# Optimization experiments

Measured on AMD Instinct MI355X. Metric: run time of the kernel, lower is better.

Reference implementation:

```python
import jax, jax.numpy as jnp
import numpy as np

B, T, A = 4096, 32, 3
HID, D, N, K = 1024, 128, 16, 4096
FLAT = T * A            # 96
LAT = N * D             # 2048
COMMIT = 0.25


def setup_inputs() -> dict:
    key = jax.random.key(0)
    ks = jax.random.split(key, 14)
    s = 0.02
    return {
        "actions": jax.random.normal(ks[0], (B, T, A), jnp.float32),
        # encoder: FLAT -> HID -> HID -> N*D
        "e_w1": jax.random.normal(ks[1], (FLAT, HID), jnp.float32) * s,
        "e_b1": jnp.zeros((HID,), jnp.float32),
        "e_w2": jax.random.normal(ks[2], (HID, HID), jnp.float32) * s,
        "e_b2": jnp.zeros((HID,), jnp.float32),
        "e_w3": jax.random.normal(ks[3], (HID, LAT), jnp.float32) * s,
        "e_b3": jnp.zeros((LAT,), jnp.float32),
        # codebook init: uniform(-1/K, 1/K) as in torch init
        "codebook": jax.random.uniform(ks[4], (K, D), jnp.float32, -1.0 / K, 1.0 / K),
        # decoder: N*D -> HID -> HID -> FLAT
        "d_w1": jax.random.normal(ks[5], (LAT, HID), jnp.float32) * s,
        "d_b1": jnp.zeros((HID,), jnp.float32),
        "d_w2": jax.random.normal(ks[6], (HID, HID), jnp.float32) * s,
        "d_b2": jnp.zeros((HID,), jnp.float32),
        "d_w3": jax.random.normal(ks[7], (HID, FLAT), jnp.float32) * s,
        "d_b3": jnp.zeros((FLAT,), jnp.float32),
    }


def reference(actions, e_w1, e_b1, e_w2, e_b2, e_w3, e_b3, codebook,
              d_w1, d_b1, d_w2, d_b2, d_w3, d_b3):
    sg = jax.lax.stop_gradient
    b = actions.shape[0]
    # encode: [B, T*A] -> [B, N, D]
    flat = actions.reshape(b, FLAT)
    h = jax.nn.silu(flat @ e_w1 + e_b1)
    h = jax.nn.silu(h @ e_w2 + e_b2)
    latents = (h @ e_w3 + e_b3).reshape(b, N, D)
    # nearest-code search: [B*N, K] squared distances
    fl = latents.reshape(b * N, D)
    dist = (fl * fl).sum(1, keepdims=True) + (codebook * codebook).sum(1)[None, :] - 2.0 * (fl @ codebook.T)
    indices = jnp.argmin(dist, axis=1).reshape(b, N)
    quantized = codebook[indices]                      # [B, N, D]
    codebook_loss = jnp.mean((quantized - sg(latents)) ** 2)
    commitment_loss = jnp.mean((latents - sg(quantized)) ** 2)
    vq_loss = codebook_loss + COMMIT * commitment_loss
    q_st = latents + sg(quantized - latents)           # straight-through
    # decode
    g = jax.nn.silu(q_st.reshape(b, LAT) @ d_w1 + d_b1)
    g = jax.nn.silu(g @ d_w2 + d_b2)
    recon = (g @ d_w3 + d_b3).reshape(b, T, A)
    recon_loss = jnp.mean((recon - actions) ** 2)
    loss = recon_loss + vq_loss
    return recon, indices, vq_loss, recon_loss, loss
```

## Files before the change

### kernel.cpp

```cpp
#include <hip/hip_runtime.h>
#include <hip/hip_bf16.h>

#define DD 128

__global__ void plant_diag(float val, float* out) {
    if (threadIdx.x == 0 && blockIdx.x == 0) out[0] = val;
}

__global__ void zero_acc(double* acc) {
    if (threadIdx.x == 0 && blockIdx.x == 0) { acc[0] = 0.0; acc[1] = 0.0; }
}

__device__ __forceinline__ float silu_np(float x) {
    float e = (float)exp(-(double)x);
    float u = 1.0f + e;
    float v = 1.0f / u;
    return x * v;
}

template <bool SILU>
__global__ __launch_bounds__(256) void gemm_db(const float* __restrict__ A,
                                               const float* __restrict__ W,
                                               const float* __restrict__ bias,
                                               float* __restrict__ C,
                                               int M, int N, int K) {
    __shared__ __align__(16) float As[128][36];
    __shared__ __align__(16) float Ws[32][68];
    const int t = threadIdx.x;
    const int tx = t & 15, ty = t >> 4;
    const int bm = blockIdx.y * 128, bn = blockIdx.x * 64;

    float acc[8][4];
#pragma unroll
    for (int i = 0; i < 8; ++i)
#pragma unroll
        for (int j = 0; j < 4; ++j) acc[i][j] = 0.0f;

    const int nPanels = (K + 31) / 32;
    float ra[16], rw[8];

    {
        const int k0 = 0;
#pragma unroll
        for (int it = 0; it < 16; ++it) {
            int e = t + 256 * it;
            int m = e >> 5, kk = e & 31;
            int mm = bm + m; if (mm >= M) mm = M - 1;
            int kc = k0 + kk;
            ra[it] = (kc < K) ? A[(size_t)mm * K + kc] : 0.0f;
        }
#pragma unroll
        for (int it = 0; it < 8; ++it) {
            int e = t + 256 * it;
            int r = e >> 6, c = e & 63;
            int n = bn + c;
            int kr = k0 + r;
            rw[it] = (kr < K && n < N) ? W[(size_t)kr * N + n] : 0.0f;
        }
    }

    for (int p = 0; p < nPanels; ++p) {
        __syncthreads();
#pragma unroll
        for (int it = 0; it < 16; ++it) {
            int e = t + 256 * it;
            As[e >> 5][e & 31] = ra[it];
        }
#pragma unroll
        for (int it = 0; it < 8; ++it) {
            int e = t + 256 * it;
            Ws[e >> 6][e & 63] = rw[it];
        }
        __syncthreads();

        if (p + 1 < nPanels) {
            const int k0 = (p + 1) * 32;
#pragma unroll
            for (int it = 0; it < 16; ++it) {
                int e = t + 256 * it;
                int m = e >> 5, kk = e & 31;
                int mm = bm + m; if (mm >= M) mm = M - 1;
                int kc = k0 + kk;
                ra[it] = (kc < K) ? A[(size_t)mm * K + kc] : 0.0f;
            }
#pragma unroll
            for (int it = 0; it < 8; ++it) {
                int e = t + 256 * it;
                int r = e >> 6, c = e & 63;
                int n = bn + c;
                int kr = k0 + r;
                rw[it] = (kr < K && n < N) ? W[(size_t)kr * N + n] : 0.0f;
            }
        }

#pragma unroll
        for (int kq = 0; kq < 8; ++kq) {
            float4 a4[8], w4[4];
#pragma unroll
            for (int i = 0; i < 8; ++i)
                a4[i] = *(const float4*)&As[ty + 16 * i][4 * kq];
#pragma unroll
            for (int q = 0; q < 4; ++q)
                w4[q] = *(const float4*)&Ws[4 * kq + q][4 * tx];
#pragma unroll
            for (int q = 0; q < 4; ++q) {
                const float wv[4] = {w4[q].x, w4[q].y, w4[q].z, w4[q].w};
#pragma unroll
                for (int i = 0; i < 8; ++i) {
                    const float av = ((const float*)&a4[i])[q];
#pragma unroll
                    for (int j = 0; j < 4; ++j)
                        acc[i][j] = fmaf(av, wv[j], acc[i][j]);
                }
            }
        }
    }

#pragma unroll
    for (int i = 0; i < 8; ++i) {
        int m = bm + ty + 16 * i;
#pragma unroll
        for (int j = 0; j < 4; ++j) {
            int n = bn + 4 * tx + j;
            if (m < M && n < N) {
                float x = acc[i][j] + bias[n];
                if (SILU) x = silu_np(x);
                C[(size_t)m * N + n] = x;
            }
        }
    }
}

__device__ __forceinline__ float pairwise128_sq(const float* __restrict__ x, int stride) {
    float r0 = x[0*stride]*x[0*stride], r1 = x[1*stride]*x[1*stride],
          r2 = x[2*stride]*x[2*stride], r3 = x[3*stride]*x[3*stride],
          r4 = x[4*stride]*x[4*stride], r5 = x[5*stride]*x[5*stride],
          r6 = x[6*stride]*x[6*stride], r7 = x[7*stride]*x[7*stride];
    for (int i = 8; i < 128; i += 8) {
        r0 += x[(i+0)*stride]*x[(i+0)*stride];
        r1 += x[(i+1)*stride]*x[(i+1)*stride];
        r2 += x[(i+2)*stride]*x[(i+2)*stride];
        r3 += x[(i+3)*stride]*x[(i+3)*stride];
        r4 += x[(i+4)*stride]*x[(i+4)*stride];
        r5 += x[(i+5)*stride]*x[(i+5)*stride];
        r6 += x[(i+6)*stride]*x[(i+6)*stride];
        r7 += x[(i+7)*stride]*x[(i+7)*stride];
    }
    return ((r0 + r1) + (r2 + r3)) + ((r4 + r5) + (r6 + r7));
}

__global__ void code_t2(const float* __restrict__ cb, float* __restrict__ t2, int K) {
    int k = blockIdx.x * 256 + threadIdx.x;
    if (k >= K) return;
    t2[k] = pairwise128_sq(cb + (size_t)k * DD, 1);
}

#define VQT_ROWS 128
#define VQT_CP   128
#define VQT_LT   132

__global__ __launch_bounds__(512, 2) void vq_t84(const float* __restrict__ lat,
                                                 const float* __restrict__ cb,
                                                 const float* __restrict__ t2,
                                                 float* __restrict__ pbv,
                                                 int* __restrict__ pbk,
                                                 int K, int rows_total) {
    __shared__ __align__(16) float Ls[VQT_ROWS][VQT_LT];
    __shared__ __align__(16) float Cs[VQT_CP][VQT_LT];
    __shared__ float T1s[VQT_ROWS];
    __shared__ float bwv[8][VQT_ROWS];
    __shared__ int   bwk[8][VQT_ROWS];

    const int t = threadIdx.x;
    const int tx = t & 15, ty = t >> 4;
    const int wave = t >> 6, lane = t & 63;
    const int r0 = blockIdx.x * VQT_ROWS;

#pragma unroll
    for (int it = 0; it < 8; ++it) {
        int g = t + 512 * it;
        int r = g >> 5, dq = g & 31;
        int rr = r0 + r; if (rr >= rows_total) rr = rows_total - 1;
        const float4 lv = *(const float4*)(lat + (size_t)rr * DD + 4 * dq);
        *(float4*)&Ls[r][4 * dq] = lv;
    }
    __syncthreads();

    if (t < VQT_ROWS) {
        const float* xr = &Ls[t][0];
        float4 q0 = *(const float4*)&xr[0];
        float4 q1 = *(const float4*)&xr[4];
        float a0 = q0.x*q0.x, a1 = q0.y*q0.y, a2 = q0.z*q0.z, a3 = q0.w*q0.w;
        float a4 = q1.x*q1.x, a5 = q1.y*q1.y, a6 = q1.z*q1.z, a7 = q1.w*q1.w;
#pragma unroll
        for (int i = 1; i < 16; ++i) {
            q0 = *(const float4*)&xr[8 * i];
            q1 = *(const float4*)&xr[8 * i + 4];
            a0 += q0.x*q0.x; a1 += q0.y*q0.y; a2 += q0.z*q0.z; a3 += q0.w*q0.w;
            a4 += q1.x*q1.x; a5 += q1.y*q1.y; a6 += q1.z*q1.z; a7 += q1.w*q1.w;
        }
        T1s[t] = ((a0 + a1) + (a2 + a3)) + ((a4 + a5) + (a6 + a7));
    }
    __syncthreads();

    float t1r[8];
#pragma unroll
    for (int i = 0; i < 8; ++i) t1r[i] = T1s[tx + 16 * i];

    float bestv[8]; int bestk[8];
#pragma unroll
    for (int i = 0; i < 8; ++i) { bestv[i] = 3.4e38f; bestk[i] = 0; }

    const int NPAN = K / VQT_CP;
#pragma unroll 1
    for (int p = 0; p < NPAN; ++p) {
        const float* src = cb + (size_t)p * VQT_CP * DD;
#pragma unroll
        for (int it = 0; it < 8; ++it) {
            int g = t + 512 * it;
            int cr = g >> 5, dq = g & 31;
            const float4 cv = *(const float4*)(src + (size_t)cr * DD + 4 * dq);
            *(float4*)&Cs[cr][4 * dq] = cv;
        }
        __syncthreads();

        const int kp = p * VQT_CP;
        float t2v[4];
#pragma unroll
        for (int j = 0; j < 4; ++j) t2v[j] = t2[kp + ty + 32 * j];

        float s[8][4];
#pragma unroll
        for (int i = 0; i < 8; ++i)
#pragma unroll
            for (int j = 0; j < 4; ++j) s[i][j] = 0.0f;

#pragma unroll 2
        for (int dq = 0; dq < 32; ++dq) {
            const float4 ca0 = *(const float4*)&Cs[ty     ][4 * dq];
            const float4 ca1 = *(const float4*)&Cs[ty + 32][4 * dq];
            const float4 ca2 = *(const float4*)&Cs[ty + 64][4 * dq];
            const float4 ca3 = *(const float4*)&Cs[ty + 96][4 * dq];
#pragma unroll
            for (int i = 0; i < 8; ++i) {
                const float4 la = *(const float4*)&Ls[tx + 16 * i][4 * dq];
                s[i][0] = fmaf(la.x, ca0.x, s[i][0]);
                s[i][0] = fmaf(la.y, ca0.y, s[i][0]);
                s[i][0] = fmaf(la.z, ca0.z, s[i][0]);
                s[i][0] = fmaf(la.w, ca0.w, s[i][0]);
                s[i][1] = fmaf(la.x, ca1.x, s[i][1]);
                s[i][1] = fmaf(la.y, ca1.y, s[i][1]);
                s[i][1] = fmaf(la.z, ca1.z, s[i][1]);
                s[i][1] = fmaf(la.w, ca1.w, s[i][1]);
                s[i][2] = fmaf(la.x, ca2.x, s[i][2]);
                s[i][2] = fmaf(la.y, ca2.y, s[i][2]);
                s[i][2] = fmaf(la.z, ca2.z, s[i][2]);
                s[i][2] = fmaf(la.w, ca2.w, s[i][2]);
                s[i][3] = fmaf(la.x, ca3.x, s[i][3]);
                s[i][3] = fmaf(la.y, ca3.y, s[i][3]);
                s[i][3] = fmaf(la.z, ca3.z, s[i][3]);
                s[i][3] = fmaf(la.w, ca3.w, s[i][3]);
            }
        }

#pragma unroll
        for (int i = 0; i < 8; ++i) {
            const float tt1 = t1r[i];
#pragma unroll
            for (int j = 0; j < 4; ++j) {
                const int c = kp + ty + 32 * j;
                const float dist = (tt1 + t2v[j]) - 2.0f * s[i][j];
                if (dist < bestv[i]) { bestv[i] = dist; bestk[i] = c; }
            }
        }
        __syncthreads();
    }

#pragma unroll
    for (int off = 16; off <= 32; off <<= 1) {
#pragma unroll
        for (int i = 0; i < 8; ++i) {
            float vv = __shfl_xor(bestv[i], off);
            int kk = __shfl_xor(bestk[i], off);
            if (vv < bestv[i] || (vv == bestv[i] && kk < bestk[i])) {
                bestv[i] = vv; bestk[i] = kk;
            }
        }
    }
    if (lane < 16) {
#pragma unroll
        for (int i = 0; i < 8; ++i) {
            bwv[wave][tx + 16 * i] = bestv[i];
            bwk[wave][tx + 16 * i] = bestk[i];
        }
    }
    __syncthreads();
    if (t < VQT_ROWS) {
        float bv = bwv[0][t]; int bk = bwk[0][t];
#pragma unroll
        for (int w = 1; w < 8; ++w) {
            float v = bwv[w][t]; int k = bwk[w][t];
            if (v < bv || (v == bv && k < bk)) { bv = v; bk = k; }
        }
        if (r0 + t < rows_total) {
            pbv[r0 + t] = bv;
            pbk[r0 + t] = bk;
        }
    }
}

__global__ __launch_bounds__(512) void vq_np4(const float* __restrict__ lat,
                                              const float* __restrict__ cb,
                                              const float* __restrict__ t2,
                                              float* __restrict__ pbv,
                                              int* __restrict__ pbk,
                                              int K, int Kc, int rows_total) {
    __shared__ __align__(16) float Ls[128][68];
    __shared__ __align__(16) float Cs[128][68];
    __shared__ float T1s[64];
    __shared__ float T2s[64];
    __shared__ float bwv[8][68];
    __shared__ int   bwk[8][68];

    const int t = threadIdx.x;
    const int tx = t & 15, ty = t >> 4;
    const int wave = t >> 6, lane = t & 63;
    const int r0 = blockIdx.x * 64;
    const int kbeg = blockIdx.y * Kc;
    const int kend = kbeg + Kc;

#pragma unroll
    for (int it = 0; it < 4; ++it) {
        int g = t + 512 * it;
        int row = g >> 5, dq = g & 31;
        int rr = r0 + row; if (rr >= rows_total) rr = rows_total - 1;
        const float4 v = *(const float4*)(lat + (size_t)rr * DD + 4 * dq);
        Ls[4*dq+0][row] = v.x; Ls[4*dq+1][row] = v.y;
        Ls[4*dq+2][row] = v.z; Ls[4*dq+3][row] = v.w;
    }
    __syncthreads();
    if (t < 64) T1s[t] = pairwise128_sq(&Ls[0][t], 68);

    float bestv[4]; int bestk[4];
#pragma unroll
    for (int r = 0; r < 4; ++r) { bestv[r] = 3.4e38f; bestk[r] = 0; }

    float4 pc[4];
    float pt2 = 0.0f;
#pragma unroll
    for (int it = 0; it < 4; ++it) {
        int g = t + 512 * it;
        int c = g >> 5, dq = g & 31;
        int cc = kbeg + c; if (cc >= K) cc = K - 1;
        pc[it] = *(const float4*)(cb + (size_t)cc * DD + 4 * dq);
    }
    if (t < 64) { int cc = kbeg + t; if (cc >= K) cc = K - 1; pt2 = t2[cc]; }

    for (int k0 = kbeg; k0 < kend; k0 += 64) {
        __syncthreads();
#pragma unroll
        for (int it = 0; it < 4; ++it) {
            int g = t + 512 * it;
            int c = g >> 5, dq = g & 31;
            Cs[4*dq+0][c] = pc[it].x; Cs[4*dq+1][c] = pc[it].y;
            Cs[4*dq+2][c] = pc[it].z; Cs[4*dq+3][c] = pc[it].w;
        }
        if (t < 64) T2s[t] = pt2;
        __syncthreads();

        if (k0 + 64 < kend) {
            const int kn = k0 + 64;
#pragma unroll
            for (int it = 0; it < 4; ++it) {
                int g = t + 512 * it;
                int c = g >> 5, dq = g & 31;
                int cc = kn + c; if (cc >= K) cc = K - 1;
                pc[it] = *(const float4*)(cb + (size_t)cc * DD + 4 * dq);
            }
            if (t < 64) { int cc = kn + t; if (cc >= K) cc = K - 1; pt2 = t2[cc]; }
        }

        float s[4][2];
#pragma unroll
        for (int r = 0; r < 4; ++r) { s[r][0] = 0.0f; s[r][1] = 0.0f; }

#pragma unroll 8
        for (int d = 0; d < 128; ++d) {
            const float4 a4 = *(const float4*)&Ls[d][4 * tx];
            const float2 c2 = *(const float2*)&Cs[d][2 * ty];
            const float av[4] = {a4.x, a4.y, a4.z, a4.w};
#pragma unroll
            for (int r = 0; r < 4; ++r) {
                s[r][0] = fmaf(av[r], c2.x, s[r][0]);
                s[r][1] = fmaf(av[r], c2.y, s[r][1]);
            }
        }

#pragma unroll
        for (int r = 0; r < 4; ++r) {
            const float t1 = T1s[4 * tx + r];
#pragma unroll
            for (int j = 0; j < 2; ++j) {
                int kc = k0 + 2 * ty + j;
                float dist = (t1 + T2s[2 * ty + j]) - 2.0f * s[r][j];
                if (kc < K && dist < bestv[r]) { bestv[r] = dist; bestk[r] = kc; }
            }
        }
    }

#pragma unroll
    for (int off = 16; off <= 32; off <<= 1) {
#pragma unroll
        for (int r = 0; r < 4; ++r) {
            float vv = __shfl_xor(bestv[r], off);
            int kk = __shfl_xor(bestk[r], off);
            if (vv < bestv[r] || (vv == bestv[r] && kk < bestk[r])) {
                bestv[r] = vv; bestk[r] = kk;
            }
        }
    }
    if (lane < 16) {
#pragma unroll
        for (int r = 0; r < 4; ++r) {
            bwv[wave][4 * lane + r] = bestv[r];
            bwk[wave][4 * lane + r] = bestk[r];
        }
    }
    __syncthreads();
    if (t < 64) {
        float bv = bwv[0][t]; int bk = bwk[0][t];
#pragma unroll
        for (int w = 1; w < 8; ++w) {
            float v = bwv[w][t]; int k = bwk[w][t];
            if (v < bv || (v == bv && k < bk)) { bv = v; bk = k; }
        }
        if (r0 + t < rows_total) {
            size_t o = (size_t)blockIdx.y * rows_total + (r0 + t);
            pbv[o] = bv;
            pbk[o] = bk;
        }
    }
}

__global__ __launch_bounds__(256) void vq_combine(const float* __restrict__ pbv,
                                                  const int* __restrict__ pbk,
                                                  int S, int rows,
                                                  int* __restrict__ indices,
                                                  double* __restrict__ acc) {
    int r = blockIdx.x * 256 + threadIdx.x;
    float bv = 3.4e38f; int bk = 0;
    if (r < rows) {
        for (int s = 0; s < S; ++s) {
            float v = pbv[(size_t)s * rows + r];
            int k = pbk[(size_t)s * rows + r];
            if (v < bv) { bv = v; bk = k; }
        }
        indices[r] = bk;
    }
    __shared__ double red[256];
    red[threadIdx.x] = (r < rows) ? (double)bv : 0.0;
    __syncthreads();
    for (int s = 128; s > 0; s >>= 1) {
        if (threadIdx.x < s) red[threadIdx.x] += red[threadIdx.x + s];
        __syncthreads();
    }
    if (threadIdx.x == 0) atomicAdd(acc, red[0]);
}

__global__ void q_gather(const int* __restrict__ idx, const float* __restrict__ cb,
                         float* __restrict__ Q, int count, int nlat) {
    int gid = blockIdx.x * 256 + threadIdx.x;
    if (gid >= count) return;
    int m = gid >> 11;
    int j = gid & 2047;
    int code = idx[m * nlat + (j >> 7)];
    Q[gid] = cb[((size_t)code << 7) + (j & 127)];
}

__global__ __launch_bounds__(256) void recon_out(const float* __restrict__ recon,
                                                 const float* __restrict__ actions,
                                                 float* __restrict__ out,
                                                 double* __restrict__ acc, int count) {
    int gid = blockIdx.x * 256 + threadIdx.x;
    double sq = 0.0;
    if (gid < count) {
        float rv = recon[gid];
        float av = actions[gid];
        double diff = (double)rv - (double)av;
        out[gid] = rv;
        sq = diff * diff;
    }
    __shared__ double red[256];
    red[threadIdx.x] = sq;
    __syncthreads();
    for (int s = 128; s > 0; s >>= 1) {
        if (threadIdx.x < s) red[threadIdx.x] += red[threadIdx.x + s];
        __syncthreads();
    }
    if (threadIdx.x == 0) atomicAdd(acc + 1, red[0]);
}

__global__ void idx_out(const int* __restrict__ idx, float* __restrict__ out, int count) {
    int gid = blockIdx.x * 256 + threadIdx.x;
    if (gid < count) out[gid] = (float)idx[gid];
}

__global__ void finalize(const double* __restrict__ acc, float* __restrict__ out,
                         double vq_den, double rec_den) {
    double vq = 1.25 * acc[0] / vq_den;
    double rl = acc[1] / rec_den;
    out[0] = (float)vq;
    out[1] = (float)rl;
    out[2] = (float)(rl + vq);
}

static inline int ceildiv(int a, int b) { return (a + b - 1) / b; }

extern "C" void kernel_launch(void* const* d_in, const int* in_sizes, int n_in,
                              void* d_out, int out_size, void* d_ws, size_t ws_size,
                              hipStream_t stream) {
    const float* actions = (const float*)d_in[0];
    const float* e_w1 = (const float*)d_in[1];
    const float* e_b1 = (const float*)d_in[2];
    const float* e_w2 = (const float*)d_in[3];
    const float* e_b2 = (const float*)d_in[4];
    const float* e_w3 = (const float*)d_in[5];
    const float* e_b3 = (const float*)d_in[6];
    const float* cb   = (const float*)d_in[7];
    const float* d_w1 = (const float*)d_in[8];
    const float* d_b1 = (const float*)d_in[9];
    const float* d_w2 = (const float*)d_in[10];
    const float* d_b2 = (const float*)d_in[11];
    const float* d_w3 = (const float*)d_in[12];
    const float* d_b3 = (const float*)d_in[13];
    float* out = (float*)d_out;

    const int FLAT = in_sizes[13];
    const int B    = in_sizes[0] / FLAT;
    const int HID  = in_sizes[2];
    const int LAT  = in_sizes[6];
    const int K    = in_sizes[7] / DD;
    const int NL   = LAT / DD;

    const bool tiled = (K % VQT_CP == 0);
    const int S = tiled ? 1 : ((K % 256 == 0) ? 4 : 1);
    const int Kc = K / S;

    int CHUNK = B;
    auto need = [&](int ch) -> size_t {
        return (size_t)ch * HID * 4 * 2 + (size_t)ch * LAT * 4 * 2
             + (size_t)ch * HID * 4 * 2 + (size_t)ch * FLAT * 4
             + (size_t)K * 4 + 64 + (size_t)B * NL * 4
             + (size_t)ch * NL * S * 8;
    };
    while (CHUNK > 16 && need(CHUNK) > ws_size) CHUNK >>= 1;
    if (need(CHUNK) > ws_size) {
        plant_diag<<<1, 64, 0, stream>>>(2222.0f, out);
        return;
    }
    const int NCHUNK = ceildiv(B, CHUNK);

    char* ws = (char*)d_ws;
    size_t off = 0;
    float* h1c  = (float*)(ws + off); off += (size_t)CHUNK * HID * 4;
    float* h2c  = (float*)(ws + off); off += (size_t)CHUNK * HID * 4;
    float* latc = (float*)(ws + off); off += (size_t)CHUNK * LAT * 4;
    float* Qc   = (float*)(ws + off); off += (size_t)CHUNK * LAT * 4;
    float* g1c  = (float*)(ws + off); off += (size_t)CHUNK * HID * 4;
    float* g2c  = (float*)(ws + off); off += (size_t)CHUNK * HID * 4;
    float* recc = (float*)(ws + off); off += (size_t)CHUNK * FLAT * 4;
    float* t2   = (float*)(ws + off); off += (size_t)K * 4;
    double* acc = (double*)(ws + off); off += 64;
    int*   idx  = (int*)(ws + off);   off += (size_t)B * NL * 4;
    float* pbv  = (float*)(ws + off); off += (size_t)CHUNK * NL * S * 4;
    int*   pbk  = (int*)(ws + off);

    zero_acc<<<1, 64, 0, stream>>>(acc);
    code_t2<<<ceildiv(K, 256), 256, 0, stream>>>(cb, t2, K);

    for (int c = 0; c < NCHUNK; ++c) {
        const int r0 = c * CHUNK;
        const int cbR = (B - r0 < CHUNK) ? (B - r0) : CHUNK;
        const float* act_c = actions + (size_t)r0 * FLAT;
        int* idx_c = idx + (size_t)r0 * NL;
        const int rows = cbR * NL;

        gemm_db<true><<<dim3(ceildiv(HID, 64), ceildiv(cbR, 128)), 256, 0, stream>>>(
            act_c, e_w1, e_b1, h1c, cbR, HID, FLAT);
        gemm_db<true><<<dim3(ceildiv(HID, 64), ceildiv(cbR, 128)), 256, 0, stream>>>(
            h1c, e_w2, e_b2, h2c, cbR, HID, HID);
        gemm_db<false><<<dim3(ceildiv(LAT, 64), ceildiv(cbR, 128)), 256, 0, stream>>>(
            h2c, e_w3, e_b3, latc, cbR, LAT, HID);

        if (tiled) {
            vq_t84<<<ceildiv(rows, VQT_ROWS), 512, 0, stream>>>(
                latc, cb, t2, pbv, pbk, K, rows);
        } else {
            vq_np4<<<dim3(ceildiv(rows, 64), S), 512, 0, stream>>>(
                latc, cb, t2, pbv, pbk, K, Kc, rows);
        }
        vq_combine<<<ceildiv(rows, 256), 256, 0, stream>>>(pbv, pbk, S, rows, idx_c, acc);

        q_gather<<<ceildiv(cbR * LAT, 256), 256, 0, stream>>>(idx_c, cb, Qc, cbR * LAT, NL);
        gemm_db<true><<<dim3(ceildiv(HID, 64), ceildiv(cbR, 128)), 256, 0, stream>>>(
            Qc, d_w1, d_b1, g1c, cbR, HID, LAT);
        gemm_db<true><<<dim3(ceildiv(HID, 64), ceildiv(cbR, 128)), 256, 0, stream>>>(
            g1c, d_w2, d_b2, g2c, cbR, HID, HID);
        gemm_db<false><<<dim3(ceildiv(FLAT, 64), ceildiv(cbR, 128)), 256, 0, stream>>>(
            g2c, d_w3, d_b3, recc, cbR, FLAT, HID);

        recon_out<<<ceildiv(cbR * FLAT, 256), 256, 0, stream>>>(
            recc, act_c, out + (size_t)r0 * FLAT, acc, cbR * FLAT);
    }

    idx_out<<<ceildiv(B * NL, 256), 256, 0, stream>>>(idx, out + (size_t)B * FLAT, B * NL);
    finalize<<<1, 1, 0, stream>>>(acc, out + (size_t)B * FLAT + (size_t)B * NL,
                                  (double)B * NL * DD, (double)B * FLAT);
}
```

Baseline: 1.897 ms.

## Read weights and codebook directly from global memory instead of LDS staging

The GEMM kernel stops staging the weight panel in shared memory: each thread loads its float4 weight values straight from global memory inside the inner loop, with a scalar fallback at edges. The VQ distance kernel is replaced by a variant that gives each thread 8 consecutive codes, reads codebook rows directly from global memory (relying on cache), and drops the per-panel shared-memory codebook tile and its barriers. The aim is to remove LDS store traffic and synchronisation. The cost is more global/L2 load traffic with poorer coalescing, since each thread reads a different codebook row, plus higher register pressure from the 8x8 accumulator.

```diff
diff --git a/kernel.cpp b/kernel.cpp
--- a/kernel.cpp
+++ b/kernel.cpp
@@ -25,10 +25,11 @@
                                                float* __restrict__ C,
                                                int M, int N, int K) {
     __shared__ __align__(16) float As[128][36];
-    __shared__ __align__(16) float Ws[32][68];
     const int t = threadIdx.x;
     const int tx = t & 15, ty = t >> 4;
     const int bm = blockIdx.y * 128, bn = blockIdx.x * 64;
+    const int n4 = bn + 4 * tx;
+    const bool wfull = (n4 + 3 < N);
 
     float acc[8][4];
 #pragma unroll
@@ -37,7 +38,7 @@
         for (int j = 0; j < 4; ++j) acc[i][j] = 0.0f;
 
     const int nPanels = (K + 31) / 32;
-    float ra[16], rw[8];
+    float ra[16];
 
     {
         const int k0 = 0;
@@ -49,14 +50,6 @@
             int kc = k0 + kk;
             ra[it] = (kc < K) ? A[(size_t)mm * K + kc] : 0.0f;
         }
-#pragma unroll
-        for (int it = 0; it < 8; ++it) {
-            int e = t + 256 * it;
-            int r = e >> 6, c = e & 63;
-            int n = bn + c;
-            int kr = k0 + r;
-            rw[it] = (kr < K && n < N) ? W[(size_t)kr * N + n] : 0.0f;
-        }
     }
 
     for (int p = 0; p < nPanels; ++p) {
@@ -65,11 +58,6 @@
         for (int it = 0; it < 16; ++it) {
             int e = t + 256 * it;
             As[e >> 5][e & 31] = ra[it];
-        }
-#pragma unroll
-        for (int it = 0; it < 8; ++it) {
-            int e = t + 256 * it;
-            Ws[e >> 6][e & 63] = rw[it];
         }
         __syncthreads();
 
@@ -83,16 +71,9 @@
                 int kc = k0 + kk;
                 ra[it] = (kc < K) ? A[(size_t)mm * K + kc] : 0.0f;
             }
-#pragma unroll
-            for (int it = 0; it < 8; ++it) {
-                int e = t + 256 * it;
-                int r = e >> 6, c = e & 63;
-                int n = bn + c;
-                int kr = k0 + r;
-                rw[it] = (kr < K && n < N) ? W[(size_t)kr * N + n] : 0.0f;
-            }
-        }
-
+        }
+
+        const int kp0 = 32 * p;
 #pragma unroll
         for (int kq = 0; kq < 8; ++kq) {
             float4 a4[8], w4[4];
@@ -100,8 +81,18 @@
             for (int i = 0; i < 8; ++i)
                 a4[i] = *(const float4*)&As[ty + 16 * i][4 * kq];
 #pragma unroll
-            for (int q = 0; q < 4; ++q)
-                w4[q] = *(const float4*)&Ws[4 * kq + q][4 * tx];
+            for (int q = 0; q < 4; ++q) {
+                const int kr = kp0 + 4 * kq + q;
+                if (wfull && kr < K) {
+                    w4[q] = *(const float4*)(W + (size_t)kr * N + n4);
+                } else {
+                    float e0 = (kr < K && n4 + 0 < N) ? W[(size_t)kr * N + n4 + 0] : 0.0f;
+                    float e1 = (kr < K && n4 + 1 < N) ? W[(size_t)kr * N + n4 + 1] : 0.0f;
+                    float e2 = (kr < K && n4 + 2 < N) ? W[(size_t)kr * N + n4 + 2] : 0.0f;
+                    float e3 = (kr < K && n4 + 3 < N) ? W[(size_t)kr * N + n4 + 3] : 0.0f;
+                    w4[q] = make_float4(e0, e1, e2, e3);
+                }
+            }
 #pragma unroll
             for (int q = 0; q < 4; ++q) {
                 const float wv[4] = {w4[q].x, w4[q].y, w4[q].z, w4[q].w};
@@ -155,26 +146,25 @@
     t2[k] = pairwise128_sq(cb + (size_t)k * DD, 1);
 }
 
-#define VQT_ROWS 128
-#define VQT_CP   128
-#define VQT_LT   132
-
-__global__ __launch_bounds__(512, 2) void vq_t84(const float* __restrict__ lat,
-                                                 const float* __restrict__ cb,
-                                                 const float* __restrict__ t2,
-                                                 float* __restrict__ pbv,
-                                                 int* __restrict__ pbk,
-                                                 int K, int rows_total) {
-    __shared__ __align__(16) float Ls[VQT_ROWS][VQT_LT];
-    __shared__ __align__(16) float Cs[VQT_CP][VQT_LT];
-    __shared__ float T1s[VQT_ROWS];
-    __shared__ float bwv[8][VQT_ROWS];
-    __shared__ int   bwk[8][VQT_ROWS];
+#define VQG_ROWS 128
+#define VQG_CPP  256
+#define VQG_LT   132
+
+__global__ __launch_bounds__(512) void vq_g88(const float* __restrict__ lat,
+                                              const float* __restrict__ cb,
+                                              const float* __restrict__ t2,
+                                              float* __restrict__ pbv,
+                                              int* __restrict__ pbk,
+                                              int K, int rows_total) {
+    __shared__ __align__(16) float Ls[VQG_ROWS][VQG_LT];
+    __shared__ float T1s[VQG_ROWS];
+    __shared__ float bwv[8][VQG_ROWS];
+    __shared__ int   bwk[8][VQG_ROWS];
 
     const int t = threadIdx.x;
     const int tx = t & 15, ty = t >> 4;
     const int wave = t >> 6, lane = t & 63;
-    const int r0 = blockIdx.x * VQT_ROWS;
+    const int r0 = blockIdx.x * VQG_ROWS;
 
 #pragma unroll
     for (int it = 0; it < 8; ++it) {
@@ -186,7 +176,7 @@
     }
     __syncthreads();
 
-    if (t < VQT_ROWS) {
+    if (t < VQG_ROWS) {
         const float* xr = &Ls[t][0];
         float4 q0 = *(const float4*)&xr[0];
         float4 q1 = *(const float4*)&xr[4];
@@ -211,55 +201,38 @@
 #pragma unroll
     for (int i = 0; i < 8; ++i) { bestv[i] = 3.4e38f; bestk[i] = 0; }
 
-    const int NPAN = K / VQT_CP;
+    const int NP = K / VQG_CPP;
 #pragma unroll 1
-    for (int p = 0; p < NPAN; ++p) {
-        const float* src = cb + (size_t)p * VQT_CP * DD;
-#pragma unroll
-        for (int it = 0; it < 8; ++it) {
-            int g = t + 512 * it;
-            int cr = g >> 5, dq = g & 31;
-            const float4 cv = *(const float4*)(src + (size_t)cr * DD + 4 * dq);
-            *(float4*)&Cs[cr][4 * dq] = cv;
-        }
-        __syncthreads();
-
-        const int kp = p * VQT_CP;
-        float t2v[4];
-#pragma unroll
-        for (int j = 0; j < 4; ++j) t2v[j] = t2[kp + ty + 32 * j];
-
-        float s[8][4];
+    for (int p = 0; p < NP; ++p) {
+        const int kp = p * VQG_CPP;
+        const int cbase = kp + 8 * ty;
+        const float* cp0 = cb + (size_t)cbase * DD;
+        float t2v[8];
+#pragma unroll
+        for (int j = 0; j < 8; ++j) t2v[j] = t2[cbase + j];
+
+        float s[8][8];
 #pragma unroll
         for (int i = 0; i < 8; ++i)
 #pragma unroll
-            for (int j = 0; j < 4; ++j) s[i][j] = 0.0f;
-
-#pragma unroll 2
+            for (int j = 0; j < 8; ++j) s[i][j] = 0.0f;
+
+#pragma unroll 4
         for (int dq = 0; dq < 32; ++dq) {
-            const float4 ca0 = *(const float4*)&Cs[ty     ][4 * dq];
-            const float4 ca1 = *(const float4*)&Cs[ty + 32][4 * dq];
-            const float4 ca2 = *(const float4*)&Cs[ty + 64][4 * dq];
-            const float4 ca3 = *(const float4*)&Cs[ty + 96][4 * dq];
+            float4 ca[8];
+#pragma unroll
+            for (int j = 0; j < 8; ++j)
+                ca[j] = *(const float4*)(cp0 + (size_t)j * DD + 4 * dq);
 #pragma unroll
             for (int i = 0; i < 8; ++i) {
                 const float4 la = *(const float4*)&Ls[tx + 16 * i][4 * dq];
-                s[i][0] = fmaf(la.x, ca0.x, s[i][0]);
-                s[i][0] = fmaf(la.y, ca0.y, s[i][0]);
-                s[i][0] = fmaf(la.z, ca0.z, s[i][0]);
-                s[i][0] = fmaf(la.w, ca0.w, s[i][0]);
-                s[i][1] = fmaf(la.x, ca1.x, s[i][1]);
-                s[i][1] = fmaf(la.y, ca1.y, s[i][1]);
-                s[i][1] = fmaf(la.z, ca1.z, s[i][1]);
-                s[i][1] = fmaf(la.w, ca1.w, s[i][1]);
-                s[i][2] = fmaf(la.x, ca2.x, s[i][2]);
-                s[i][2] = fmaf(la.y, ca2.y, s[i][2]);
-                s[i][2] = fmaf(la.z, ca2.z, s[i][2]);
-                s[i][2] = fmaf(la.w, ca2.w, s[i][2]);
-                s[i][3] = fmaf(la.x, ca3.x, s[i][3]);
-                s[i][3] = fmaf(la.y, ca3.y, s[i][3]);
-                s[i][3] = fmaf(la.z, ca3.z, s[i][3]);
-                s[i][3] = fmaf(la.w, ca3.w, s[i][3]);
+#pragma unroll
+                for (int j = 0; j < 8; ++j) {
+                    s[i][j] = fmaf(la.x, ca[j].x, s[i][j]);
+                    s[i][j] = fmaf(la.y, ca[j].y, s[i][j]);
+                    s[i][j] = fmaf(la.z, ca[j].z, s[i][j]);
+                    s[i][j] = fmaf(la.w, ca[j].w, s[i][j]);
+                }
             }
         }
 
@@ -267,13 +240,12 @@
         for (int i = 0; i < 8; ++i) {
             const float tt1 = t1r[i];
 #pragma unroll
-            for (int j = 0; j < 4; ++j) {
-                const int c = kp + ty + 32 * j;
+            for (int j = 0; j < 8; ++j) {
+                const int c = cbase + j;
                 const float dist = (tt1 + t2v[j]) - 2.0f * s[i][j];
                 if (dist < bestv[i]) { bestv[i] = dist; bestk[i] = c; }
             }
         }
-        __syncthreads();
     }
 
 #pragma unroll
@@ -295,7 +267,7 @@
         }
     }
     __syncthreads();
-    if (t < VQT_ROWS) {
+    if (t < VQG_ROWS) {
         float bv = bwv[0][t]; int bk = bwk[0][t];
 #pragma unroll
         for (int w = 1; w < 8; ++w) {
@@ -542,9 +514,9 @@
     const int K    = in_sizes[7] / DD;
     const int NL   = LAT / DD;
 
-    const bool tiled = (K % VQT_CP == 0);
-    const int S = tiled ? 1 : ((K % 256 == 0) ? 4 : 1);
-    const int Kc = K / S;
+    const bool g88 = (K % VQG_CPP == 0);
+    const int S = 1;
+    const int Kc = K;
 
     int CHUNK = B;
     auto need = [&](int ch) -> size_t {
@@ -592,8 +564,8 @@
         gemm_db<false><<<dim3(ceildiv(LAT, 64), ceildiv(cbR, 128)), 256, 0, stream>>>(
             h2c, e_w3, e_b3, latc, cbR, LAT, HID);
 
-        if (tiled) {
-            vq_t84<<<ceildiv(rows, VQT_ROWS), 512, 0, stream>>>(
+        if (g88) {
+            vq_g88<<<ceildiv(rows, VQG_ROWS), 512, 0, stream>>>(
                 latc, cb, t2, pbv, pbk, K, rows);
         } else {
             vq_np4<<<dim3(ceildiv(rows, 64), S), 512, 0, stream>>>(
```

After: 7.059 ms. 3.72x slower.
